# Optimization experiments

Hardware: AMD Instinct MI355X
Metric: run time of the kernel (lower is better)

## Reference

```python
import jax, jax.numpy as jnp
import numpy as np

SAMPLE_RATE = 48000
MIX = 0.5
DELAYS_SEC = [0.0297, 0.0371, 0.0411, 0.0437, 0.0533, 0.0617, 0.0731, 0.0797]
DELAYS = [int(d * SAMPLE_RATE) for d in DELAYS_SEC]  # integer sample delays
N = len(DELAYS)
T = 8388608  # ~175 s of mono audio at 48 kHz


def setup_inputs() -> dict:
    key = jax.random.key(0)
    k1, k2, k3 = jax.random.split(key, 3)
    input_sig = jax.random.normal(k1, (1, T), dtype=jnp.float32)
    feedback_gain = jax.random.uniform(k2, (N,), dtype=jnp.float32)
    # orthogonal mix matrix via QR of a random Gaussian, as in the module's __init__
    rm = np.asarray(jax.random.normal(k3, (N, N), dtype=jnp.float32))
    q, _ = np.linalg.qr(rm)
    orthogonal_matrix = jnp.asarray(q, dtype=jnp.float32)
    return {"input_sig": input_sig, "feedback_gain": feedback_gain,
            "orthogonal_matrix": orthogonal_matrix}


def reference(input_sig, feedback_gain, orthogonal_matrix):
    x = input_sig[0]  # [T]
    # Delay buffers start at zero, so each delay line's output is the input
    # shifted right by `d` samples and zero-padded at the front.
    shifted = jnp.stack(
        [jnp.concatenate([jnp.zeros((d,), x.dtype), x[: x.shape[0] - d]]) for d in DELAYS],
        axis=0)  # [N, T]
    # sum_j (Q @ (g[:,None]*shifted))[j] == (ones @ Q) * g  dotted with shifted rows
    combined = (jnp.sum(orthogonal_matrix, axis=0) * feedback_gain)  # [N]
    wet = jnp.einsum('n,nt->t', combined, shifted)[None, :]  # [1, T]
    out = wet * MIX + input_sig * (1.0 - MIX)
    out = out / jnp.max(jnp.abs(out))
    return out
```

## Files before the change

### kernel.cpp

```cpp
#include <hip/hip_runtime.h>

#define T_LEN 8388608
#define CHUNK 4096
#define HALO  3840
#define LDSF  (HALO + CHUNK)
#define NBLK  (T_LEN / CHUNK)

#define D0 1425
#define D1 1780
#define D2 1972
#define D3 2097
#define D4 2558
#define D5 2961
#define D6 3508
#define D7 3825

typedef float floatx4 __attribute__((ext_vector_type(4)));

__device__ __forceinline__ int swz(int b) {
    return (b & 7) * (NBLK / 8) + (b >> 3);
}

__device__ __forceinline__ void load_odd(const float* q, float* v) {
    float  a  = q[0];
    float2 b  = *(const float2*)(q + 1);
    float  c  = q[3];
    v[0] = a; v[1] = b.x; v[2] = b.y; v[3] = c;
}

__device__ __forceinline__ float4 quad_fir(const float* __restrict__ p,
                                           const float* __restrict__ c) {
    float4 dry = *(const float4*)(p);
    float4 t1  = *(const float4*)(p - D1);
    float4 t2  = *(const float4*)(p - D2);
    float4 t6  = *(const float4*)(p - D6);
    float2 t4a = *(const float2*)(p - D4);
    float2 t4b = *(const float2*)(p - D4 + 2);
    float t0v[4], t3v[4], t5v[4], t7v[4];
    load_odd(p - D0, t0v);
    load_odd(p - D3, t3v);
    load_odd(p - D5, t5v);
    load_odd(p - D7, t7v);
    float t4v[4] = {t4a.x, t4a.y, t4b.x, t4b.y};

    float4 o;
#pragma unroll
    for (int k = 0; k < 4; ++k) {
        float wet = 0.f;
        wet = fmaf(c[0], t0v[k],      wet);
        wet = fmaf(c[1], (&t1.x)[k],  wet);
        wet = fmaf(c[2], (&t2.x)[k],  wet);
        wet = fmaf(c[3], t3v[k],      wet);
        wet = fmaf(c[4], t4v[k],      wet);
        wet = fmaf(c[5], t5v[k],      wet);
        wet = fmaf(c[6], (&t6.x)[k],  wet);
        wet = fmaf(c[7], t7v[k],      wet);
        (&o.x)[k] = fmaf(0.5f, wet, 0.5f * (&dry.x)[k]);
    }
    return o;
}

__device__ __forceinline__ void stage(const float* __restrict__ x, float* smem,
                                      int blk, int tid) {
    const long gs = (long)blk * CHUNK - HALO;
    for (int v4 = tid; v4 < LDSF / 4; v4 += 256) {
        long ga = gs + (long)v4 * 4;
        float4 val = make_float4(0.f, 0.f, 0.f, 0.f);
        if (ga >= 0) val = *(const float4*)(x + ga);
        *(float4*)(smem + v4 * 4) = val;
    }
}

__device__ __forceinline__ void load_coeffs(const float* __restrict__ g,
                                            const float* __restrict__ Q,
                                            float* csh, int tid) {
    if (tid < 8) {
        float s = 0.f;
#pragma unroll
        for (int j = 0; j < 8; ++j) s += Q[j * 8 + tid];
        csh[tid] = s * g[tid];
    }
}

__global__ __launch_bounds__(256) void fdn_max(
    const float* __restrict__ x, const float* __restrict__ g,
    const float* __restrict__ Q, float* __restrict__ slots) {
    __shared__ __align__(16) float smem[LDSF];
    __shared__ float csh[8];
    __shared__ float wmax[4];

    const int tid = threadIdx.x;
    const int blk = swz(blockIdx.x);

    load_coeffs(g, Q, csh, tid);
    stage(x, smem, blk, tid);
    __syncthreads();

    float c[8];
#pragma unroll
    for (int n = 0; n < 8; ++n) c[n] = csh[n];

    float m = 0.f;
#pragma unroll
    for (int i = 0; i < CHUNK / 1024; ++i) {
        const float* p = smem + HALO + i * 1024 + tid * 4;
        float4 o = quad_fir(p, c);
        m = fmaxf(m, fmaxf(fmaxf(fabsf(o.x), fabsf(o.y)),
                           fmaxf(fabsf(o.z), fabsf(o.w))));
    }

#pragma unroll
    for (int off = 32; off > 0; off >>= 1) m = fmaxf(m, __shfl_down(m, off, 64));
    if ((tid & 63) == 0) wmax[tid >> 6] = m;
    __syncthreads();
    if (tid == 0)
        slots[blk] = fmaxf(fmaxf(wmax[0], wmax[1]), fmaxf(wmax[2], wmax[3]));
}

__global__ __launch_bounds__(256) void fdn_write(
    const float* __restrict__ x, const float* __restrict__ g,
    const float* __restrict__ Q, const float* __restrict__ slots,
    float* __restrict__ out) {
    __shared__ __align__(16) float smem[LDSF];
    __shared__ float csh[8];
    __shared__ float wmax[4];

    const int tid = threadIdx.x;
    const int blk = swz(blockIdx.x);

    load_coeffs(g, Q, csh, tid);

    float4 s0 = *(const float4*)(slots + tid * 8);
    float4 s1 = *(const float4*)(slots + tid * 8 + 4);

    stage(x, smem, blk, tid);

    float m = fmaxf(fmaxf(fmaxf(s0.x, s0.y), fmaxf(s0.z, s0.w)),
                    fmaxf(fmaxf(s1.x, s1.y), fmaxf(s1.z, s1.w)));
#pragma unroll
    for (int off = 32; off > 0; off >>= 1) m = fmaxf(m, __shfl_down(m, off, 64));
    if ((tid & 63) == 0) wmax[tid >> 6] = m;
    __syncthreads();

    const float inv = 1.0f / fmaxf(fmaxf(wmax[0], wmax[1]),
                                   fmaxf(wmax[2], wmax[3]));
    float c[8];
#pragma unroll
    for (int n = 0; n < 8; ++n) c[n] = csh[n];

    const int base = blk * CHUNK;
#pragma unroll
    for (int i = 0; i < CHUNK / 1024; ++i) {
        const int j = i * 1024 + tid * 4;
        const float* p = smem + HALO + j;
        float4 o = quad_fir(p, c);
        floatx4 ov;
        ov.x = o.x * inv; ov.y = o.y * inv;
        ov.z = o.z * inv; ov.w = o.w * inv;
        __builtin_nontemporal_store(ov, (floatx4*)(out + base + j));
    }
}

extern "C" void kernel_launch(void* const* d_in, const int* in_sizes, int n_in,
                              void* d_out, int out_size, void* d_ws, size_t ws_size,
                              hipStream_t stream) {
    const float* x = (const float*)d_in[0];
    const float* g = (const float*)d_in[1];
    const float* Q = (const float*)d_in[2];
    float* out = (float*)d_out;
    float* slots = (float*)d_ws;

    fdn_max  <<<dim3(NBLK), dim3(256), 0, stream>>>(x, g, Q, slots);
    fdn_write<<<dim3(NBLK), dim3(256), 0, stream>>>(x, g, Q, slots, out);
}
```

Measured before the change: 107.1 us.

## Store unnormalized output in first pass and rescale in place in second

The first kernel now writes the unnormalized output to global memory as well as computing per-block maxima. The second kernel reads that output back and scales it, instead of restaging the input with its halo and recomputing the FIR. This trades the recompute and halo reload for an extra 32 MB write plus read of the output, which may cost more bandwidth than it saves. Tap loads are also changed to aligned float4 reads with register shuffling, replacing the odd-alignment scalar and float2 reads.

```diff
diff --git a/kernel.cpp b/kernel.cpp
--- a/kernel.cpp
+++ b/kernel.cpp
@@ -21,40 +21,46 @@
     return (b & 7) * (NBLK / 8) + (b >> 3);
 }
 
-__device__ __forceinline__ void load_odd(const float* q, float* v) {
-    float  a  = q[0];
-    float2 b  = *(const float2*)(q + 1);
-    float  c  = q[3];
-    v[0] = a; v[1] = b.x; v[2] = b.y; v[3] = c;
+template <int D>
+__device__ __forceinline__ void tap4(const float* __restrict__ p, float v[4]) {
+    constexpr int r = (4 - (D & 3)) & 3;
+    const float* q = p - D - r;
+    float4 w0 = *(const float4*)q;
+    if constexpr (r == 0) {
+        v[0] = w0.x; v[1] = w0.y; v[2] = w0.z; v[3] = w0.w;
+    } else {
+        float4 w1 = *(const float4*)(q + 4);
+        float w[8] = {w0.x, w0.y, w0.z, w0.w, w1.x, w1.y, w1.z, w1.w};
+#pragma unroll
+        for (int k = 0; k < 4; ++k) v[k] = w[r + k];
+    }
 }
 
 __device__ __forceinline__ float4 quad_fir(const float* __restrict__ p,
                                            const float* __restrict__ c) {
     float4 dry = *(const float4*)(p);
-    float4 t1  = *(const float4*)(p - D1);
-    float4 t2  = *(const float4*)(p - D2);
-    float4 t6  = *(const float4*)(p - D6);
-    float2 t4a = *(const float2*)(p - D4);
-    float2 t4b = *(const float2*)(p - D4 + 2);
-    float t0v[4], t3v[4], t5v[4], t7v[4];
-    load_odd(p - D0, t0v);
-    load_odd(p - D3, t3v);
-    load_odd(p - D5, t5v);
-    load_odd(p - D7, t7v);
-    float t4v[4] = {t4a.x, t4a.y, t4b.x, t4b.y};
+    float t0v[4], t1v[4], t2v[4], t3v[4], t4v[4], t5v[4], t6v[4], t7v[4];
+    tap4<D0>(p, t0v);
+    tap4<D1>(p, t1v);
+    tap4<D2>(p, t2v);
+    tap4<D3>(p, t3v);
+    tap4<D4>(p, t4v);
+    tap4<D5>(p, t5v);
+    tap4<D6>(p, t6v);
+    tap4<D7>(p, t7v);
 
     float4 o;
 #pragma unroll
     for (int k = 0; k < 4; ++k) {
         float wet = 0.f;
-        wet = fmaf(c[0], t0v[k],      wet);
-        wet = fmaf(c[1], (&t1.x)[k],  wet);
-        wet = fmaf(c[2], (&t2.x)[k],  wet);
-        wet = fmaf(c[3], t3v[k],      wet);
-        wet = fmaf(c[4], t4v[k],      wet);
-        wet = fmaf(c[5], t5v[k],      wet);
-        wet = fmaf(c[6], (&t6.x)[k],  wet);
-        wet = fmaf(c[7], t7v[k],      wet);
+        wet = fmaf(c[0], t0v[k], wet);
+        wet = fmaf(c[1], t1v[k], wet);
+        wet = fmaf(c[2], t2v[k], wet);
+        wet = fmaf(c[3], t3v[k], wet);
+        wet = fmaf(c[4], t4v[k], wet);
+        wet = fmaf(c[5], t5v[k], wet);
+        wet = fmaf(c[6], t6v[k], wet);
+        wet = fmaf(c[7], t7v[k], wet);
         (&o.x)[k] = fmaf(0.5f, wet, 0.5f * (&dry.x)[k]);
     }
     return o;
@@ -82,9 +88,10 @@
     }
 }
 
-__global__ __launch_bounds__(256) void fdn_max(
+__global__ __launch_bounds__(256) void fdn_wet(
     const float* __restrict__ x, const float* __restrict__ g,
-    const float* __restrict__ Q, float* __restrict__ slots) {
+    const float* __restrict__ Q, float* __restrict__ slots,
+    float* __restrict__ out) {
     __shared__ __align__(16) float smem[LDSF];
     __shared__ float csh[8];
     __shared__ float wmax[4];
@@ -100,13 +107,15 @@
 #pragma unroll
     for (int n = 0; n < 8; ++n) c[n] = csh[n];
 
+    const int base = blk * CHUNK;
     float m = 0.f;
 #pragma unroll
     for (int i = 0; i < CHUNK / 1024; ++i) {
-        const float* p = smem + HALO + i * 1024 + tid * 4;
-        float4 o = quad_fir(p, c);
+        const int j = i * 1024 + tid * 4;
+        float4 o = quad_fir(smem + HALO + j, c);
         m = fmaxf(m, fmaxf(fmaxf(fabsf(o.x), fabsf(o.y)),
                            fmaxf(fabsf(o.z), fabsf(o.w))));
+        *(float4*)(out + base + j) = o;
     }
 
 #pragma unroll
@@ -117,46 +126,32 @@
         slots[blk] = fmaxf(fmaxf(wmax[0], wmax[1]), fmaxf(wmax[2], wmax[3]));
 }
 
-__global__ __launch_bounds__(256) void fdn_write(
-    const float* __restrict__ x, const float* __restrict__ g,
-    const float* __restrict__ Q, const float* __restrict__ slots,
-    float* __restrict__ out) {
-    __shared__ __align__(16) float smem[LDSF];
-    __shared__ float csh[8];
+__global__ __launch_bounds__(256) void fdn_scale(
+    const float* __restrict__ slots, float* __restrict__ out) {
     __shared__ float wmax[4];
 
     const int tid = threadIdx.x;
     const int blk = swz(blockIdx.x);
 
-    load_coeffs(g, Q, csh, tid);
-
     float4 s0 = *(const float4*)(slots + tid * 8);
     float4 s1 = *(const float4*)(slots + tid * 8 + 4);
-
-    stage(x, smem, blk, tid);
-
     float m = fmaxf(fmaxf(fmaxf(s0.x, s0.y), fmaxf(s0.z, s0.w)),
                     fmaxf(fmaxf(s1.x, s1.y), fmaxf(s1.z, s1.w)));
 #pragma unroll
     for (int off = 32; off > 0; off >>= 1) m = fmaxf(m, __shfl_down(m, off, 64));
     if ((tid & 63) == 0) wmax[tid >> 6] = m;
     __syncthreads();
-
     const float inv = 1.0f / fmaxf(fmaxf(wmax[0], wmax[1]),
                                    fmaxf(wmax[2], wmax[3]));
-    float c[8];
-#pragma unroll
-    for (int n = 0; n < 8; ++n) c[n] = csh[n];
 
     const int base = blk * CHUNK;
 #pragma unroll
     for (int i = 0; i < CHUNK / 1024; ++i) {
         const int j = i * 1024 + tid * 4;
-        const float* p = smem + HALO + j;
-        float4 o = quad_fir(p, c);
+        float4 v = *(const float4*)(out + base + j);
         floatx4 ov;
-        ov.x = o.x * inv; ov.y = o.y * inv;
-        ov.z = o.z * inv; ov.w = o.w * inv;
+        ov.x = v.x * inv; ov.y = v.y * inv;
+        ov.z = v.z * inv; ov.w = v.w * inv;
         __builtin_nontemporal_store(ov, (floatx4*)(out + base + j));
     }
 }
@@ -170,6 +165,6 @@
     float* out = (float*)d_out;
     float* slots = (float*)d_ws;
 
-    fdn_max  <<<dim3(NBLK), dim3(256), 0, stream>>>(x, g, Q, slots);
-    fdn_write<<<dim3(NBLK), dim3(256), 0, stream>>>(x, g, Q, slots, out);
+    fdn_wet  <<<dim3(NBLK), dim3(256), 0, stream>>>(x, g, Q, slots, out);
+    fdn_scale<<<dim3(NBLK), dim3(256), 0, stream>>>(slots, out);
 }
```

After: 111.2 us. +3.8%, slower.
